# Kernel optimization log

Hardware: AMD Instinct MI355X
Metric: run time of the kernel (lower is better)

Reference implementation:

```python
import jax, jax.numpy as jnp
import numpy as np

N, E, G = 50000, 500000, 8
IN, HID, OUT, NC, H = 256, 128, 64, 10, 2
NPG = N // G  # nodes per graph
NEG_SLOPE = 0.2


def setup_inputs() -> dict:
    key = jax.random.key(0)
    ks = jax.random.split(key, 24)
    x = jax.random.normal(ks[0], (N, IN), jnp.float32)
    # edges constrained to stay within each graph, no self-loops
    src = jax.random.randint(ks[1], (E,), 0, N)
    base = (src // NPG) * NPG
    off = jax.random.randint(ks[2], (E,), 1, NPG)
    dst = base + (src - base + off) % NPG
    edge_index = jnp.stack([src, dst], axis=0).astype(jnp.int32)
    edge_attr = jax.random.uniform(ks[3], (E, 1), jnp.float32)
    batch = jnp.repeat(jnp.arange(G, dtype=jnp.int32), NPG)
    y = jax.random.randint(ks[4], (N,), 0, NC).astype(jnp.int32)

    s = 0.1
    p = {
        'W1': jax.random.normal(ks[5], (IN, H * HID), jnp.float32) * s,
        'att_src1': jax.random.normal(ks[6], (H, HID), jnp.float32) * s,
        'att_dst1': jax.random.normal(ks[7], (H, HID), jnp.float32) * s,
        'We1': jax.random.normal(ks[8], (1, H * HID), jnp.float32) * s,
        'att_edge1': jax.random.normal(ks[9], (H, HID), jnp.float32) * s,
        'b1': jnp.zeros((HID,), jnp.float32),
        'W2': jax.random.normal(ks[10], (HID, H * OUT), jnp.float32) * s,
        'att_src2': jax.random.normal(ks[11], (H, OUT), jnp.float32) * s,
        'att_dst2': jax.random.normal(ks[12], (H, OUT), jnp.float32) * s,
        'We2': jax.random.normal(ks[13], (1, H * OUT), jnp.float32) * s,
        'att_edge2': jax.random.normal(ks[14], (H, OUT), jnp.float32) * s,
        'b2': jnp.zeros((OUT,), jnp.float32),
        'Wc': jax.random.normal(ks[15], (OUT, NC), jnp.float32) * s,
        'bc': jnp.zeros((NC,), jnp.float32),
    }
    return dict(x=x, edge_index=edge_index, edge_attr=edge_attr, batch=batch, y=y, **p)


def _gat_layer(x, src, dst, eattr, W, a_src, a_dst, We, a_e, b, n_nodes, C):
    # PyG GATConv: heads=H, concat=False (mean over heads), edge_dim features.
    xp = (x @ W).reshape(n_nodes, H, C)                    # [N,H,C]
    al_s = jnp.einsum('nhc,hc->nh', xp, a_src)             # [N,H]
    al_d = jnp.einsum('nhc,hc->nh', xp, a_dst)
    ef = (eattr @ We).reshape(-1, H, C)                    # [E,H,C]
    al_e = jnp.einsum('ehc,hc->eh', ef, a_e)               # [E,H]
    alpha = jax.nn.leaky_relu(al_s[src] + al_d[dst] + al_e, NEG_SLOPE)
    # edge softmax grouped by destination (every dst has a self-loop -> no empty segs)
    m = jax.ops.segment_max(alpha, dst, num_segments=n_nodes)
    ex = jnp.exp(alpha - m[dst])
    denom = jax.ops.segment_sum(ex, dst, num_segments=n_nodes)
    w = ex / (denom[dst] + 1e-16)                          # [E,H]
    msg = xp[src] * w[:, :, None]                          # [E,H,C]
    out = jax.ops.segment_sum(msg, dst, num_segments=n_nodes)  # [N,H,C]
    return out.mean(axis=1) + b


def reference(x, edge_index, edge_attr, batch, y,
              W1, att_src1, att_dst1, We1, att_edge1, b1,
              W2, att_src2, att_dst2, We2, att_edge2, b2,
              Wc, bc):
    src, dst = edge_index[0], edge_index[1]
    # add self-loops; edge_attr fill = per-graph mean (as in the per-graph loop)
    g = batch[src]
    cnt = jax.ops.segment_sum(jnp.ones_like(edge_attr[:, 0]), g, num_segments=G)
    mean_attr = jax.ops.segment_sum(edge_attr, g, num_segments=G) / cnt[:, None]
    loop_attr = mean_attr[batch]                           # [N,1]
    ar = jnp.arange(N, dtype=src.dtype)
    src_a = jnp.concatenate([src, ar])
    dst_a = jnp.concatenate([dst, ar])
    ea = jnp.concatenate([edge_attr, loop_attr], axis=0)

    h = _gat_layer(x, src_a, dst_a, ea, W1, att_src1, att_dst1, We1, att_edge1, b1, N, HID)
    h = jax.nn.relu(h)
    h = _gat_layer(h, src_a, dst_a, ea, W2, att_src2, att_dst2, We2, att_edge2, b2, N, OUT)
    pred = h @ Wc + bc                                     # [N,NC]
    return pred, y
```

## Files before the change

kernel.cpp:

```cpp
#include <hip/hip_runtime.h>
#include <hip/hip_bf16.h>
#include <cstdint>
#include <cstddef>

#define N_NODES 50000
#define N_EDGES 500000
#define EA_EDGES 550000
#define NPG 6250
#define G_GRAPHS 8
#define IN_DIM 256
#define HID_DIM 128
#define OUT_DIM 64
#define NCLS 10
#define NEG_SLOPE 0.2f

typedef __attribute__((ext_vector_type(8))) short short8v;
typedef __attribute__((ext_vector_type(4))) float f32x4;

__device__ __forceinline__ unsigned short f2bf(float f) {
  __hip_bfloat16 h = __float2bfloat16(f);
  unsigned short u;
  __builtin_memcpy(&u, &h, 2);
  return u;
}
__device__ __forceinline__ float bf2f(unsigned short u) {
  return __uint_as_float(((unsigned)u) << 16);
}

__global__ void k_sums_degree(const int* __restrict__ src, const int* __restrict__ dst,
                              const float* __restrict__ eattr,
                              float* __restrict__ sums, float* __restrict__ cnts,
                              int* __restrict__ deg) {
  __shared__ float ls[G_GRAPHS], lc[G_GRAPHS];
  if (threadIdx.x < G_GRAPHS) { ls[threadIdx.x] = 0.f; lc[threadIdx.x] = 0.f; }
  __syncthreads();
  int stride = gridDim.x * blockDim.x;
  for (int e = blockIdx.x * blockDim.x + threadIdx.x; e < EA_EDGES; e += stride) {
    if (e < N_EDGES) {
      int g = src[e] / NPG;
      atomicAdd(&ls[g], eattr[e]);
      atomicAdd(&lc[g], 1.f);
      atomicAdd(&deg[dst[e]], 1);
    } else {
      atomicAdd(&deg[e - N_EDGES], 1);
    }
  }
  __syncthreads();
  if (threadIdx.x < G_GRAPHS) {
    atomicAdd(&sums[threadIdx.x], ls[threadIdx.x]);
    atomicAdd(&cnts[threadIdx.x], lc[threadIdx.x]);
  }
}

__global__ void k_prep(const float* __restrict__ sums, const float* __restrict__ cnts,
                       float* __restrict__ mean,
                       const float* __restrict__ We1, const float* __restrict__ ae1,
                       const float* __restrict__ We2, const float* __restrict__ ae2,
                       float* __restrict__ ce) {
  if (threadIdx.x == 0 && blockIdx.x == 0) {
    for (int g = 0; g < G_GRAPHS; ++g) mean[g] = sums[g] / cnts[g];
    for (int h = 0; h < 2; ++h) {
      float s = 0.f;
      for (int c = 0; c < HID_DIM; ++c) s += We1[h * HID_DIM + c] * ae1[h * HID_DIM + c];
      ce[h] = s;
    }
    for (int h = 0; h < 2; ++h) {
      float s = 0.f;
      for (int c = 0; c < OUT_DIM; ++c) s += We2[h * OUT_DIM + c] * ae2[h * OUT_DIM + c];
      ce[2 + h] = s;
    }
  }
}

__global__ void k_scan1(const int* __restrict__ deg, int* __restrict__ rowptr,
                        int* __restrict__ bsum, int n) {
  __shared__ int sm[1024];
  int tid = threadIdx.x;
  int i = blockIdx.x * 1024 + tid;
  int v = (i < n) ? deg[i] : 0;
  sm[tid] = v;
  __syncthreads();
  for (int off = 1; off < 1024; off <<= 1) {
    int t = (tid >= off) ? sm[tid - off] : 0;
    __syncthreads();
    if (tid >= off) sm[tid] += t;
    __syncthreads();
  }
  if (i < n) rowptr[i] = sm[tid] - v;
  if (tid == 1023) bsum[blockIdx.x] = sm[1023];
}

__global__ void k_scan2(int* __restrict__ bsum, int* __restrict__ rowptr, int nb, int n) {
  if (threadIdx.x == 0 && blockIdx.x == 0) {
    int run = 0;
    for (int i = 0; i < nb; ++i) { int v = bsum[i]; bsum[i] = run; run += v; }
    rowptr[n] = run;
  }
}

__global__ void k_scan3(int* __restrict__ rowptr, int* __restrict__ cursor,
                        const int* __restrict__ bsum, int n) {
  int i = blockIdx.x * blockDim.x + threadIdx.x;
  if (i < n) {
    int r = rowptr[i] + bsum[i >> 10];
    rowptr[i] = r;
    cursor[i] = r;
  }
}

__global__ void k_fill(const int* __restrict__ src, const int* __restrict__ dst,
                       const float* __restrict__ eattr, const float* __restrict__ mean,
                       int* __restrict__ cursor, int2* __restrict__ csr) {
  int e = blockIdx.x * blockDim.x + threadIdx.x;
  if (e >= EA_EDGES) return;
  int s, d; float a;
  if (e < N_EDGES) { s = src[e]; d = dst[e]; a = eattr[e]; }
  else { int i = e - N_EDGES; s = i; d = i; a = mean[i / NPG]; }
  int p = atomicAdd(&cursor[d], 1);
  csr[p] = make_int2(s, __float_as_int(a));
}

__global__ void k_cast_bf16(const float* __restrict__ in, unsigned short* __restrict__ out, int n8) {
  int i = blockIdx.x * blockDim.x + threadIdx.x;
  if (i >= n8) return;
  float4 a = *(const float4*)(in + (size_t)i * 8);
  float4 b = *(const float4*)(in + (size_t)i * 8 + 4);
  uint4 o;
  o.x = (unsigned)f2bf(a.x) | ((unsigned)f2bf(a.y) << 16);
  o.y = (unsigned)f2bf(a.z) | ((unsigned)f2bf(a.w) << 16);
  o.z = (unsigned)f2bf(b.x) | ((unsigned)f2bf(b.y) << 16);
  o.w = (unsigned)f2bf(b.z) | ((unsigned)f2bf(b.w) << 16);
  *(uint4*)(out + (size_t)i * 8) = o;
}

__global__ void k_cast_t(const float* __restrict__ W, unsigned short* __restrict__ Wt,
                         int K, int N) {
  int i = blockIdx.x * blockDim.x + threadIdx.x;
  if (i >= K * N) return;
  int k = i / N, n = i - k * N;
  Wt[(size_t)n * K + k] = f2bf(W[i]);
}

template <int K>
__global__ __launch_bounds__(256) void k_gemm_mfma(const unsigned short* __restrict__ A,
                                                   const unsigned short* __restrict__ Bt,
                                                   unsigned short* __restrict__ C,
                                                   int M, int Nout,
                                                   const float* __restrict__ a_src,
                                                   const float* __restrict__ a_dst,
                                                   float* __restrict__ als,
                                                   float* __restrict__ ald) {
  constexpr int BM = 128, BN = 128, BK = 64;
  __shared__ __attribute__((aligned(16))) unsigned short As[BM * BK];
  __shared__ __attribute__((aligned(16))) unsigned short Bs[BN * BK];
  const int tid = threadIdx.x;
  const int lane = tid & 63;
  const int wid = tid >> 6;
  const int wr = wid >> 1, wc = wid & 1;
  const int r0 = blockIdx.y * BM, c0 = blockIdx.x * BN;
  f32x4 acc[4][4] = {};

  for (int k0 = 0; k0 < K; k0 += BK) {
#pragma unroll
    for (int i = 0; i < 4; ++i) {
      int c = tid + i * 256;
      int row = c >> 3, kc = c & 7;
      int gr = r0 + row;
      uint4 v = make_uint4(0, 0, 0, 0);
      if (gr < M) v = *(const uint4*)(A + (size_t)gr * K + k0 + kc * 8);
      int boff = (row * 128 + kc * 16) ^ ((row & 7) << 4);
      *(uint4*)((char*)As + boff) = v;
    }
#pragma unroll
    for (int i = 0; i < 4; ++i) {
      int c = tid + i * 256;
      int row = c >> 3, kc = c & 7;
      uint4 v = *(const uint4*)(Bt + (size_t)(c0 + row) * K + k0 + kc * 8);
      int boff = (row * 128 + kc * 16) ^ ((row & 7) << 4);
      *(uint4*)((char*)Bs + boff) = v;
    }
    __syncthreads();
#pragma unroll
    for (int ks = 0; ks < 2; ++ks) {
      short8v a[4], b[4];
#pragma unroll
      for (int mi = 0; mi < 4; ++mi) {
        int row = wr * 64 + mi * 16 + (lane & 15);
        int boff = (row * 128 + ks * 64 + (lane >> 4) * 16) ^ ((row & 7) << 4);
        a[mi] = *(const short8v*)((const char*)As + boff);
      }
#pragma unroll
      for (int ni = 0; ni < 4; ++ni) {
        int row = wc * 64 + ni * 16 + (lane & 15);
        int boff = (row * 128 + ks * 64 + (lane >> 4) * 16) ^ ((row & 7) << 4);
        b[ni] = *(const short8v*)((const char*)Bs + boff);
      }
#pragma unroll
      for (int mi = 0; mi < 4; ++mi)
#pragma unroll
        for (int ni = 0; ni < 4; ++ni)
          acc[mi][ni] = __builtin_amdgcn_mfma_f32_16x16x32_bf16(a[mi], b[ni], acc[mi][ni], 0, 0, 0);
    }
    __syncthreads();
  }

#pragma unroll
  for (int mi = 0; mi < 4; ++mi) {
#pragma unroll
    for (int r = 0; r < 4; ++r) {
      int row = r0 + wr * 64 + mi * 16 + (lane >> 4) * 4 + r;
      if (row < M) {
#pragma unroll
        for (int ni = 0; ni < 4; ++ni) {
          int col = c0 + wc * 64 + ni * 16 + (lane & 15);
          C[(size_t)row * Nout + col] = f2bf(acc[mi][ni][r]);
        }
      }
    }
  }

  {
    int headc = (c0 + wc * 64) / (Nout >> 1);
    float asv[4], adv[4];
#pragma unroll
    for (int ni = 0; ni < 4; ++ni) {
      int col = c0 + wc * 64 + ni * 16 + (lane & 15);
      asv[ni] = a_src[col];
      adv[ni] = a_dst[col];
    }
#pragma unroll
    for (int mi = 0; mi < 4; ++mi) {
#pragma unroll
      for (int r = 0; r < 4; ++r) {
        float ps = 0.f, pd = 0.f;
#pragma unroll
        for (int ni = 0; ni < 4; ++ni) {
          ps += acc[mi][ni][r] * asv[ni];
          pd += acc[mi][ni][r] * adv[ni];
        }
#pragma unroll
        for (int off = 1; off < 16; off <<= 1) {
          ps += __shfl_xor(ps, off);
          pd += __shfl_xor(pd, off);
        }
        int row = r0 + wr * 64 + mi * 16 + (lane >> 4) * 4 + r;
        if ((lane & 15) == 0 && row < M) {
          atomicAdd(&als[2 * row + headc], ps);
          atomicAdd(&ald[2 * row + headc], pd);
        }
      }
    }
  }
}

template <int C, bool RELU, bool BF16OUT>
__global__ void k_aggregate(const unsigned short* __restrict__ xp,
                            const float* __restrict__ als, const float* __restrict__ ald,
                            const int* __restrict__ rowptr, const int2* __restrict__ csr,
                            const float* __restrict__ ce,
                            const float* __restrict__ bias, void* __restrict__ outv) {
  constexpr int TC = 2 * C;
  constexpr int VPL = TC / 64;
  int lane = threadIdx.x & 63;
  int wid = threadIdx.x >> 6;
  int local = (blockIdx.x >> 3) * 4 + wid;
  if (local >= NPG) return;
  int node = (blockIdx.x & 7) * NPG + local;
  int p0 = rowptr[node], p1 = rowptr[node + 1];
  int deg = p1 - p0;
  int half = lane >> 5;
  int sub = lane & 31;
  float ald_m = ald[2 * node + half];
  float ce_m = ce[half];
  float m = -1e30f, den = 0.f;
  float acc[VPL];
#pragma unroll
  for (int k = 0; k < VPL; ++k) acc[k] = 0.f;

  for (int base = 0; base < deg; base += 32) {
    int nE = min(32, deg - base);
    float a = -1e30f;
    int s = 0;
    float w = 0.f;
    if (sub < nE) {
      int2 md = csr[p0 + base + sub];
      s = md.x;
      float ea = __int_as_float(md.y);
      float l = als[2 * s + half] + ald_m + ce_m * ea;
      a = (l > 0.f) ? l : NEG_SLOPE * l;
    }
    float cm = a;
#pragma unroll
    for (int off = 1; off < 32; off <<= 1) cm = fmaxf(cm, __shfl_xor(cm, off));
    float nm = fmaxf(m, cm);
    float cs = __expf(m - nm);
    m = nm;
    if (sub < nE) w = __expf(a - m);
    float ws = w;
#pragma unroll
    for (int off = 1; off < 32; off <<= 1) ws += __shfl_xor(ws, off);
    den = den * cs + ws;
#pragma unroll
    for (int k = 0; k < VPL; ++k) acc[k] *= cs;
    for (int e0 = 0; e0 < nE; e0 += 8) {
      int se[8]; float wh[8];
#pragma unroll
      for (int j = 0; j < 8; ++j) {
        int e = e0 + j;
        se[j] = __shfl(s, e);
        wh[j] = __shfl(w, e | (lane & 32));
      }
      if (VPL == 4) {
        ushort4 u[8];
#pragma unroll
        for (int j = 0; j < 8; ++j)
          u[j] = *(const ushort4*)(xp + (size_t)se[j] * TC + lane * VPL);
#pragma unroll
        for (int j = 0; j < 8; ++j) {
          acc[0] += wh[j] * bf2f(u[j].x);
          acc[1] += wh[j] * bf2f(u[j].y);
          acc[2] += wh[j] * bf2f(u[j].z);
          acc[3] += wh[j] * bf2f(u[j].w);
        }
      } else {
        ushort2 u[8];
#pragma unroll
        for (int j = 0; j < 8; ++j)
          u[j] = *(const ushort2*)(xp + (size_t)se[j] * TC + lane * VPL);
#pragma unroll
        for (int j = 0; j < 8; ++j) {
          acc[0] += wh[j] * bf2f(u[j].x);
          acc[1] += wh[j] * bf2f(u[j].y);
        }
      }
    }
  }

  float deni = 1.f / (den + 1e-16f);
  float t[VPL];
#pragma unroll
  for (int k = 0; k < VPL; ++k) {
    t[k] = acc[k] * deni;
    t[k] += __shfl_xor(t[k], 32);
  }
  if (lane < 32) {
    int c = lane * VPL;
    float v[VPL];
#pragma unroll
    for (int k = 0; k < VPL; ++k) {
      v[k] = 0.5f * t[k] + bias[c + k];
      if (RELU) v[k] = fmaxf(v[k], 0.f);
    }
    if (BF16OUT) {
      unsigned short* o = (unsigned short*)outv + (size_t)node * C + c;
      if (VPL == 4) {
        ushort4 u;
        u.x = f2bf(v[0]); u.y = f2bf(v[1]); u.z = f2bf(v[2]); u.w = f2bf(v[3]);
        *(ushort4*)o = u;
      } else {
        ushort2 u; u.x = f2bf(v[0]); u.y = f2bf(v[1]);
        *(ushort2*)o = u;
      }
    } else {
      float* o = (float*)outv + (size_t)node * C + c;
#pragma unroll
      for (int k = 0; k < VPL; ++k) o[k] = v[k];
    }
  }
}

__global__ void k_classifier(const float* __restrict__ h2, const float* __restrict__ Wc,
                             const float* __restrict__ bc, const int* __restrict__ y,
                             float* __restrict__ out) {
  __shared__ float wcs[OUT_DIM * NCLS];
  __shared__ float bcs[NCLS];
  for (int i = threadIdx.x; i < OUT_DIM * NCLS; i += blockDim.x) wcs[i] = Wc[i];
  if (threadIdx.x < NCLS) bcs[threadIdx.x] = bc[threadIdx.x];
  __syncthreads();
  int n = blockIdx.x * blockDim.x + threadIdx.x;
  if (n >= N_NODES) return;
  float acc[NCLS];
#pragma unroll
  for (int j = 0; j < NCLS; ++j) acc[j] = bcs[j];
  for (int k = 0; k < OUT_DIM; ++k) {
    float v = h2[(size_t)n * OUT_DIM + k];
#pragma unroll
    for (int j = 0; j < NCLS; ++j) acc[j] += v * wcs[k * NCLS + j];
  }
#pragma unroll
  for (int j = 0; j < NCLS; ++j) out[(size_t)n * NCLS + j] = acc[j];
  out[(size_t)N_NODES * NCLS + n] = (float)y[n];
}

extern "C" void kernel_launch(void* const* d_in, const int* in_sizes, int n_in,
                              void* d_out, int out_size, void* d_ws, size_t ws_size,
                              hipStream_t stream) {
  const float* x     = (const float*)d_in[0];
  const int*   ei    = (const int*)d_in[1];
  const float* eattr = (const float*)d_in[2];
  const int*   y     = (const int*)d_in[4];
  const float* W1  = (const float*)d_in[5];
  const float* as1 = (const float*)d_in[6];
  const float* ad1 = (const float*)d_in[7];
  const float* We1 = (const float*)d_in[8];
  const float* ae1 = (const float*)d_in[9];
  const float* b1  = (const float*)d_in[10];
  const float* W2  = (const float*)d_in[11];
  const float* as2 = (const float*)d_in[12];
  const float* ad2 = (const float*)d_in[13];
  const float* We2 = (const float*)d_in[14];
  const float* ae2 = (const float*)d_in[15];
  const float* b2  = (const float*)d_in[16];
  const float* Wc  = (const float*)d_in[17];
  const float* bc  = (const float*)d_in[18];
  float* out = (float*)d_out;

  const int* src = ei;
  const int* dst = ei + N_EDGES;

  char* wsb = (char*)d_ws;
  size_t o = 0;
  auto alloc = [&](size_t bytes) { size_t r = o; o = (o + bytes + 255) & ~(size_t)255; return r; };
  size_t o_sums   = alloc(G_GRAPHS * 4);
  size_t o_cnts   = alloc(G_GRAPHS * 4);
  size_t o_mean   = alloc(G_GRAPHS * 4);
  size_t o_ce     = alloc(4 * 4);
  size_t o_bsum   = alloc(64 * 4);
  size_t o_deg    = alloc((size_t)N_NODES * 4);
  size_t o_rowptr = alloc((size_t)(N_NODES + 1) * 4);
  size_t o_cursor = alloc((size_t)N_NODES * 4);
  size_t o_csr    = alloc((size_t)EA_EDGES * 8);
  size_t o_xb     = alloc((size_t)N_NODES * IN_DIM * 2);
  size_t o_wt1    = alloc((size_t)IN_DIM * 256 * 2);
  size_t o_wt2    = alloc((size_t)HID_DIM * 128 * 2);
  size_t o_xp     = alloc((size_t)N_NODES * 256 * 2);
  size_t o_h1b    = alloc((size_t)N_NODES * HID_DIM * 2);
  size_t o_h2     = alloc((size_t)N_NODES * OUT_DIM * 4);
  size_t o_als    = alloc((size_t)N_NODES * 2 * 4);
  size_t o_ald    = alloc((size_t)N_NODES * 2 * 4);
  (void)ws_size;

  float* sums   = (float*)(wsb + o_sums);
  float* cnts   = (float*)(wsb + o_cnts);
  float* mean   = (float*)(wsb + o_mean);
  float* ce     = (float*)(wsb + o_ce);
  int*   bsum   = (int*)(wsb + o_bsum);
  int*   deg    = (int*)(wsb + o_deg);
  int*   rowptr = (int*)(wsb + o_rowptr);
  int*   cursor = (int*)(wsb + o_cursor);
  int2*  csr    = (int2*)(wsb + o_csr);
  unsigned short* xb  = (unsigned short*)(wsb + o_xb);
  unsigned short* wt1 = (unsigned short*)(wsb + o_wt1);
  unsigned short* wt2 = (unsigned short*)(wsb + o_wt2);
  unsigned short* xp  = (unsigned short*)(wsb + o_xp);
  unsigned short* h1b = (unsigned short*)(wsb + o_h1b);
  float* h2     = (float*)(wsb + o_h2);
  float* als    = (float*)(wsb + o_als);
  float* ald    = (float*)(wsb + o_ald);
  size_t alsald_bytes = (o_ald - o_als) + (size_t)N_NODES * 2 * 4;

  hipMemsetAsync(sums, 0, G_GRAPHS * 4 * 2, stream);
  hipMemsetAsync(deg, 0, (size_t)N_NODES * 4, stream);

  k_cast_bf16<<<(N_NODES * IN_DIM / 8 + 255) / 256, 256, 0, stream>>>(x, xb, N_NODES * IN_DIM / 8);
  k_cast_t<<<(IN_DIM * 256 + 255) / 256, 256, 0, stream>>>(W1, wt1, IN_DIM, 256);
  k_cast_t<<<(HID_DIM * 128 + 255) / 256, 256, 0, stream>>>(W2, wt2, HID_DIM, 128);

  k_sums_degree<<<512, 256, 0, stream>>>(src, dst, eattr, sums, cnts, deg);
  k_prep<<<1, 64, 0, stream>>>(sums, cnts, mean, We1, ae1, We2, ae2, ce);

  int eaBlocks = (EA_EDGES + 255) / 256;
  int nScanBlocks = (N_NODES + 1023) / 1024;
  k_scan1<<<nScanBlocks, 1024, 0, stream>>>(deg, rowptr, bsum, N_NODES);
  k_scan2<<<1, 64, 0, stream>>>(bsum, rowptr, nScanBlocks, N_NODES);
  k_scan3<<<(N_NODES + 255) / 256, 256, 0, stream>>>(rowptr, cursor, bsum, N_NODES);
  k_fill<<<eaBlocks, 256, 0, stream>>>(src, dst, eattr, mean, cursor, csr);

  int aggBlocks = G_GRAPHS * ((NPG + 3) / 4);

  hipMemsetAsync(als, 0, alsald_bytes, stream);
  {
    dim3 grid(256 / 128, (N_NODES + 127) / 128);
    k_gemm_mfma<IN_DIM><<<grid, 256, 0, stream>>>(xb, wt1, xp, N_NODES, 256,
                                                  as1, ad1, als, ald);
  }
  k_aggregate<HID_DIM, true, true><<<aggBlocks, 256, 0, stream>>>(
      xp, als, ald, rowptr, csr, ce, b1, h1b);

  hipMemsetAsync(als, 0, alsald_bytes, stream);
  {
    dim3 grid(128 / 128, (N_NODES + 127) / 128);
    k_gemm_mfma<HID_DIM><<<grid, 256, 0, stream>>>(h1b, wt2, xp, N_NODES, 128,
                                                   as2, ad2, als, ald);
  }
  k_aggregate<OUT_DIM, false, false><<<aggBlocks, 256, 0, stream>>>(
      xp, als, ald, rowptr, csr, ce + 2, b2, h2);

  k_classifier<<<(N_NODES + 255) / 256, 256, 0, stream>>>(h2, Wc, bc, y, out);
}
```

Measured before the change: 333.2 us.

## Double-buffer GEMM tiles with direct global-to-LDS loads and padded row buffers

The bf16 MFMA GEMM now stages A and B tiles with global_load_lds (global memory straight into LDS) into two LDS buffers. The next k-tile loads while the current one is multiplied, and one barrier per iteration is dropped. The row bounds check on A is removed, so the input buffers are padded to M_PAD rows so the last tile reads stay in range. The padding rows are never initialised, but their outputs are masked at store. Doubling the LDS tiles raises shared-memory use per block, which may lower occupancy.

```diff
diff --git a/kernel.cpp b/kernel.cpp
--- a/kernel.cpp
+++ b/kernel.cpp
@@ -13,6 +13,7 @@
 #define OUT_DIM 64
 #define NCLS 10
 #define NEG_SLOPE 0.2f
+#define M_PAD 50048
 
 typedef __attribute__((ext_vector_type(8))) short short8v;
 typedef __attribute__((ext_vector_type(4))) float f32x4;
@@ -25,6 +26,13 @@
 }
 __device__ __forceinline__ float bf2f(unsigned short u) {
   return __uint_as_float(((unsigned)u) << 16);
+}
+
+__device__ __forceinline__ void gl_lds16(const unsigned short* g, unsigned short* l) {
+  __builtin_amdgcn_global_load_lds(
+      (const __attribute__((address_space(1))) unsigned int*)(g),
+      (__attribute__((address_space(3))) unsigned int*)(l),
+      16, 0, 0);
 }
 
 __global__ void k_sums_degree(const int* __restrict__ src, const int* __restrict__ dst,
@@ -151,8 +159,9 @@
                                                    float* __restrict__ als,
                                                    float* __restrict__ ald) {
   constexpr int BM = 128, BN = 128, BK = 64;
-  __shared__ __attribute__((aligned(16))) unsigned short As[BM * BK];
-  __shared__ __attribute__((aligned(16))) unsigned short Bs[BN * BK];
+  constexpr int TSZ = BM * BK;
+  __shared__ __attribute__((aligned(16))) unsigned short As[2 * TSZ];
+  __shared__ __attribute__((aligned(16))) unsigned short Bs[2 * TSZ];
   const int tid = threadIdx.x;
   const int lane = tid & 63;
   const int wid = tid >> 6;
@@ -160,26 +169,30 @@
   const int r0 = blockIdx.y * BM, c0 = blockIdx.x * BN;
   f32x4 acc[4][4] = {};
 
-  for (int k0 = 0; k0 < K; k0 += BK) {
+  const int srow = wid * 32 + (lane >> 3);
+  const int schunk = (lane & 7) ^ (lane >> 3);
+  const unsigned short* gA = A + (size_t)(r0 + srow) * K + schunk * 8;
+  const unsigned short* gB = Bt + (size_t)(c0 + srow) * K + schunk * 8;
+
+  auto stage = [&](int buf, int k0) {
+    unsigned short* Ab = As + buf * TSZ + wid * 2048;
+    unsigned short* Bb = Bs + buf * TSZ + wid * 2048;
 #pragma unroll
     for (int i = 0; i < 4; ++i) {
-      int c = tid + i * 256;
-      int row = c >> 3, kc = c & 7;
-      int gr = r0 + row;
-      uint4 v = make_uint4(0, 0, 0, 0);
-      if (gr < M) v = *(const uint4*)(A + (size_t)gr * K + k0 + kc * 8);
-      int boff = (row * 128 + kc * 16) ^ ((row & 7) << 4);
-      *(uint4*)((char*)As + boff) = v;
-    }
-#pragma unroll
-    for (int i = 0; i < 4; ++i) {
-      int c = tid + i * 256;
-      int row = c >> 3, kc = c & 7;
-      uint4 v = *(const uint4*)(Bt + (size_t)(c0 + row) * K + k0 + kc * 8);
-      int boff = (row * 128 + kc * 16) ^ ((row & 7) << 4);
-      *(uint4*)((char*)Bs + boff) = v;
-    }
+      gl_lds16(gA + (size_t)(i * 8) * K + k0, Ab + i * 512);
+      gl_lds16(gB + (size_t)(i * 8) * K + k0, Bb + i * 512);
+    }
+  };
+
+  constexpr int NT = K / BK;
+  int cur = 0;
+  stage(0, 0);
+#pragma unroll
+  for (int t = 0; t < NT; ++t) {
     __syncthreads();
+    if (t + 1 < NT) stage(cur ^ 1, (t + 1) * BK);
+    const char* Ab = (const char*)(As + cur * TSZ);
+    const char* Bb = (const char*)(Bs + cur * TSZ);
 #pragma unroll
     for (int ks = 0; ks < 2; ++ks) {
       short8v a[4], b[4];
@@ -187,13 +200,13 @@
       for (int mi = 0; mi < 4; ++mi) {
         int row = wr * 64 + mi * 16 + (lane & 15);
         int boff = (row * 128 + ks * 64 + (lane >> 4) * 16) ^ ((row & 7) << 4);
-        a[mi] = *(const short8v*)((const char*)As + boff);
+        a[mi] = *(const short8v*)(Ab + boff);
       }
 #pragma unroll
       for (int ni = 0; ni < 4; ++ni) {
         int row = wc * 64 + ni * 16 + (lane & 15);
         int boff = (row * 128 + ks * 64 + (lane >> 4) * 16) ^ ((row & 7) << 4);
-        b[ni] = *(const short8v*)((const char*)Bs + boff);
+        b[ni] = *(const short8v*)(Bb + boff);
       }
 #pragma unroll
       for (int mi = 0; mi < 4; ++mi)
@@ -201,7 +214,7 @@
         for (int ni = 0; ni < 4; ++ni)
           acc[mi][ni] = __builtin_amdgcn_mfma_f32_16x16x32_bf16(a[mi], b[ni], acc[mi][ni], 0, 0, 0);
     }
-    __syncthreads();
+    cur ^= 1;
   }
 
 #pragma unroll
@@ -430,11 +443,11 @@
   size_t o_rowptr = alloc((size_t)(N_NODES + 1) * 4);
   size_t o_cursor = alloc((size_t)N_NODES * 4);
   size_t o_csr    = alloc((size_t)EA_EDGES * 8);
-  size_t o_xb     = alloc((size_t)N_NODES * IN_DIM * 2);
+  size_t o_xb     = alloc((size_t)M_PAD * IN_DIM * 2);
   size_t o_wt1    = alloc((size_t)IN_DIM * 256 * 2);
   size_t o_wt2    = alloc((size_t)HID_DIM * 128 * 2);
   size_t o_xp     = alloc((size_t)N_NODES * 256 * 2);
-  size_t o_h1b    = alloc((size_t)N_NODES * HID_DIM * 2);
+  size_t o_h1b    = alloc((size_t)M_PAD * HID_DIM * 2);
   size_t o_h2     = alloc((size_t)N_NODES * OUT_DIM * 4);
   size_t o_als    = alloc((size_t)N_NODES * 2 * 4);
   size_t o_ald    = alloc((size_t)N_NODES * 2 * 4);
@@ -480,7 +493,7 @@
 
   hipMemsetAsync(als, 0, alsald_bytes, stream);
   {
-    dim3 grid(256 / 128, (N_NODES + 127) / 128);
+    dim3 grid(256 / 128, M_PAD / 128);
     k_gemm_mfma<IN_DIM><<<grid, 256, 0, stream>>>(xb, wt1, xp, N_NODES, 256,
                                                   as1, ad1, als, ald);
   }
@@ -489,7 +502,7 @@
 
   hipMemsetAsync(als, 0, alsald_bytes, stream);
   {
-    dim3 grid(128 / 128, (N_NODES + 127) / 128);
+    dim3 grid(128 / 128, M_PAD / 128);
     k_gemm_mfma<HID_DIM><<<grid, 256, 0, stream>>>(h1b, wt2, xp, N_NODES, 128,
                                                    as2, ad2, als, ald);
   }
```

Measured after the change: 333.1 us. About the same (-0.0%).
